# Kernel optimization log

Hardware: AMD Instinct MI355X
Metric: run time of the kernel (lower is better)

## Reference

```python
import jax, jax.numpy as jnp
import numpy as np

DT = 0.001          # continuous-dynamics step (dt > 0 branch)
KERNEL_SIZE = 16384 # L
P, H = 1024, 256    # d_state, d_input (= d_output)


def setup_inputs() -> dict:
    key = jax.random.key(0)
    kAr, kAi, kB, kC = jax.random.split(key, 4)
    # Continuous diagonal state matrix: real part in [strong, weak] = [-0.5, -0.01] (stable),
    # imaginary part uniform in [-pi, pi] (mimics diagonal_state_space_matrix init).
    Ar = jax.random.uniform(kAr, (P,), minval=-0.5, maxval=-0.01)
    Ai = jax.random.uniform(kAi, (P,), minval=-np.pi, maxval=np.pi)
    A = jnp.stack([Ar, Ai], axis=-1).astype(jnp.float32)            # (P, 2) view_as_real
    # B, C ~ uniform disk (radius 1): scaled complex gaussians are a fine stand-in numerically.
    B = (jax.random.normal(kB, (P, H, 2)) / np.sqrt(H)).astype(jnp.float32)   # (P, H, 2)
    C = (jax.random.normal(kC, (H, P, 2)) / np.sqrt(P)).astype(jnp.float32)   # (H, P, 2)
    return {"A": A, "B": B, "C": C}


def _as_complex(x):
    return x[..., 0] + 1j * x[..., 1]


def reference(A, B, C):
    """Vandermonde SSM kernel generation (continuous dt > 0 branch).
    Returns kernel (H, L, 2) = real view of complex kernel (H, L)."""
    Ac = _as_complex(A)   # (P,) complex
    Bc = _as_complex(B)   # (P, H)
    Cc = _as_complex(C)   # (H, P)

    # ZOH-style discretization
    A_bar = jnp.exp(Ac * DT)                               # (P,)
    B_bar = ((A_bar - 1.0) / Ac)[:, None] * Bc             # (P, H)

    # Vandermonde matrix V[p, l] = A_bar[p] ** l  (complex power == exp(l * log(a)))
    powers = jnp.arange(KERNEL_SIZE, dtype=jnp.float32)    # (L,)
    V = jnp.exp(jnp.log(A_bar)[:, None] * powers[None, :]) # (P, L)

    # W[h, p] = C[h, p] * B_bar[p, h]; kernel[h, l] = sum_p W[h, p] * V[p, l]
    W = Cc * B_bar.T                                       # (H, P)
    kernel = jnp.einsum('hp,pl->hl', W, V)                 # (H, L) complex
    return jnp.stack([kernel.real, kernel.imag], axis=-1)  # (H, L, 2) float32
```

## Files before the change

### kernel.cpp

```cpp
#include <hip/hip_runtime.h>
#include <hip/hip_fp16.h>

#define P_DIM 1024
#define H_DIM 256
#define L_DIM 16384
#define DT 0.001f
#define TWOPI 6.283185307179586f
#define WSCALE 4096.0f
#define INV_WSCALE (1.0f / 4096.0f)

#define BM 128
#define BN 128
#define BK 64
#define NTHREADS 256

typedef _Float16 f16x8 __attribute__((ext_vector_type(8)));
typedef float f32x4 __attribute__((ext_vector_type(4)));

#define GPTR(p) (const __attribute__((address_space(1))) unsigned*)(p)
#define LPTR(p) (__attribute__((address_space(3))) unsigned*)(p)

union H2U { __half2 h; unsigned u; };

__global__ __launch_bounds__(256)
void prep_kernel(const float* __restrict__ Ag, const float* __restrict__ Bg,
                 const float* __restrict__ Cg, __half* __restrict__ W2) {
    int gid = blockIdx.x * 256 + threadIdx.x;
    int h = gid >> 10, p = gid & 1023;
    float2 a = ((const float2*)Ag)[p];
    float er = __expf(a.x * DT);
    float s, c;
    __sincosf(a.y * DT, &s, &c);
    float nr = er * c - 1.0f, ni = er * s;
    float inv = 1.0f / (a.x * a.x + a.y * a.y);
    float sr = (nr * a.x + ni * a.y) * inv;
    float si = (ni * a.x - nr * a.y) * inv;
    float2 b = ((const float2*)Bg)[p * H_DIM + h];
    float2 cc = ((const float2*)Cg)[h * P_DIM + p];
    float tr = cc.x * sr - cc.y * si, ti = cc.x * si + cc.y * sr;
    float wr = (tr * b.x - ti * b.y) * WSCALE;
    float wi = (tr * b.y + ti * b.x) * WSCALE;
    ((__half2*)W2)[h * P_DIM + p] = __float22half2_rn(make_float2(wr, wi));
}

__global__ __launch_bounds__(NTHREADS)
void vand_mfma_kernel(const float* __restrict__ Ag,
                      const _Float16* __restrict__ W2,
                      float* __restrict__ out) {
    __shared__ __attribute__((aligned(16))) _Float16 As[BM * BK];
    __shared__ __attribute__((aligned(16))) _Float16 Bs[BN * BK];
    __shared__ __attribute__((aligned(16))) float2 pc[P_DIM];

    const int tid  = threadIdx.x;
    const int lane = tid & 63;
    const int w    = tid >> 6;
    const int wm   = w & 1;
    const int wn   = w >> 1;
    const int m0   = blockIdx.y * BM;
    const int nb   = blockIdx.x * BN;
    const int lb   = blockIdx.x * (BN / 2);

    #pragma unroll
    for (int i = 0; i < 4; ++i) {
        int p = i * 256 + tid;
        float2 a = ((const float2*)Ag)[p];
        pc[p] = make_float2(a.x * DT, a.y * DT * 0.15915494309189535f);
    }
    __syncthreads();

    f32x4 acc[4][4];
    #pragma unroll
    for (int mt = 0; mt < 4; ++mt)
        #pragma unroll
        for (int nt = 0; nt < 4; ++nt)
            acc[mt][nt] = (f32x4){0.f, 0.f, 0.f, 0.f};

    const int lv   = tid >> 2;
    const float fl = (float)(lb + lv);
    const int n0   = 2 * lv;
    const int qb   = tid & 3;

    for (int kk = 0; kk < 32; ++kk) {
        const int k0 = kk * BK;
        if (kk) __syncthreads();

        {
            const _Float16* gw = W2 + (size_t)(m0 + (w << 5)) * 2048 + k0;
            const int goff = (lane >> 3) * 2048 + (((lane & 7) ^ (lane >> 3)) << 3);
            _Float16* lbase = As + (w << 5) * 64;
            #pragma unroll
            for (int r = 0; r < 4; ++r) {
                __builtin_amdgcn_global_load_lds(GPTR(gw + r * 8 * 2048 + goff),
                                                 LPTR(lbase + r * 8 * 64), 16, 0, 0);
            }
        }

        #pragma unroll
        for (int i = 0; i < 4; ++i) {
            int q = qb + (i << 2);
            float4 pcv = *(const float4*)&pc[(k0 >> 1) + 2 * q];
            float mg0 = __expf(pcv.x * fl);
            float x0 = pcv.y * fl; x0 -= rintf(x0);
            float s0, c0; __sincosf(x0 * TWOPI, &s0, &c0);
            float vr0 = mg0 * c0, vi0 = mg0 * s0;
            float mg1 = __expf(pcv.z * fl);
            float x1 = pcv.w * fl; x1 -= rintf(x1);
            float s1, c1; __sincosf(x1 * TWOPI, &s1, &c1);
            float vr1 = mg1 * c1, vi1 = mg1 * s1;

            H2U a0, a1, b0, b1;
            a0.h = __float22half2_rn(make_float2(vr0, -vi0));
            a1.h = __float22half2_rn(make_float2(vr1, -vi1));
            b0.h = __float22half2_rn(make_float2(vi0, vr0));
            b1.h = __float22half2_rn(make_float2(vi1, vr1));
            int grp = q >> 1, sub = (q & 1) << 2;
            int e0 = n0 * 64 + ((grp ^ (n0 & 7)) << 3) + sub;
            int e1 = (n0 + 1) * 64 + ((grp ^ ((n0 + 1) & 7)) << 3) + sub;
            *(uint2*)(Bs + e0) = make_uint2(a0.u, a1.u);
            *(uint2*)(Bs + e1) = make_uint2(b0.u, b1.u);
        }
        __syncthreads();

        #pragma unroll
        for (int ks = 0; ks < 2; ++ks) {
            f16x8 af[4], bf[4];
            const int g = ks * 4 + (lane >> 4);
            #pragma unroll
            for (int t = 0; t < 4; ++t) {
                int m = wm * 64 + t * 16 + (lane & 15);
                af[t] = *(const f16x8*)(As + m * 64 + ((g ^ (m & 7)) << 3));
                int n = wn * 64 + t * 16 + (lane & 15);
                bf[t] = *(const f16x8*)(Bs + n * 64 + ((g ^ (n & 7)) << 3));
            }
            #pragma unroll
            for (int mt = 0; mt < 4; ++mt)
                #pragma unroll
                for (int nt = 0; nt < 4; ++nt)
                    acc[mt][nt] = __builtin_amdgcn_mfma_f32_16x16x32_f16(
                        af[mt], bf[nt], acc[mt][nt], 0, 0, 0);
        }
    }

    #pragma unroll
    for (int mt = 0; mt < 4; ++mt) {
        #pragma unroll
        for (int nt = 0; nt < 4; ++nt) {
            int h = m0 + wm * 64 + mt * 16 + ((lane >> 4) << 2);
            int n = nb + wn * 64 + nt * 16 + (lane & 15);
            #pragma unroll
            for (int r = 0; r < 4; ++r)
                out[(size_t)(h + r) * 32768 + n] = acc[mt][nt][r] * INV_WSCALE;
        }
    }
}

extern "C" void kernel_launch(void* const* d_in, const int* in_sizes, int n_in,
                              void* d_out, int out_size, void* d_ws, size_t ws_size,
                              hipStream_t stream) {
    const float* A = (const float*)d_in[0];
    const float* B = (const float*)d_in[1];
    const float* C = (const float*)d_in[2];
    float* out = (float*)d_out;
    __half* W2 = (__half*)d_ws;

    prep_kernel<<<dim3(1024), dim3(256), 0, stream>>>(A, B, C, W2);
    vand_mfma_kernel<<<dim3(L_DIM * 2 / BN, H_DIM / BM), dim3(NTHREADS), 0, stream>>>(
        A, (const _Float16*)W2, out);
}
```

Measured before the change: 115.6 us.

## Double-buffer LDS tiles, generate Vandermonde by recurrence, and tile prep transpose

The main kernel now double-buffers the A and B LDS tiles, so the next chunk's DMA and Vandermonde generation are issued before the current chunk's MFMAs, with one barrier per iteration. Each thread now computes one exp/sincos per state and derives three further consecutive powers by complex multiplication with A_bar, which reduces transcendental work per element. Launch bounds are raised to two blocks per CU. The prep kernel is restructured to load a block of B into shared memory so the transposed read is coalesced. The recurrence may accumulate rounding error, and the doubled LDS could limit occupancy.

```diff
diff --git a/kernel.cpp b/kernel.cpp
--- a/kernel.cpp
+++ b/kernel.cpp
@@ -6,13 +6,13 @@
 #define L_DIM 16384
 #define DT 0.001f
 #define TWOPI 6.283185307179586f
+#define INV2PI 0.15915494309189535f
 #define WSCALE 4096.0f
 #define INV_WSCALE (1.0f / 4096.0f)
-
 #define BM 128
 #define BN 128
 #define BK 64
-#define NTHREADS 256
+#define NT 256
 
 typedef _Float16 f16x8 __attribute__((ext_vector_type(8)));
 typedef float f32x4 __attribute__((ext_vector_type(4)));
@@ -21,52 +21,63 @@
 #define LPTR(p) (__attribute__((address_space(3))) unsigned*)(p)
 
 union H2U { __half2 h; unsigned u; };
+
+__device__ __forceinline__ float2 cmulf(float2 a, float2 b) {
+    return make_float2(a.x * b.x - a.y * b.y, a.x * b.y + a.y * b.x);
+}
 
 __global__ __launch_bounds__(256)
 void prep_kernel(const float* __restrict__ Ag, const float* __restrict__ Bg,
                  const float* __restrict__ Cg, __half* __restrict__ W2) {
-    int gid = blockIdx.x * 256 + threadIdx.x;
-    int h = gid >> 10, p = gid & 1023;
-    float2 a = ((const float2*)Ag)[p];
-    float er = __expf(a.x * DT);
-    float s, c;
-    __sincosf(a.y * DT, &s, &c);
-    float nr = er * c - 1.0f, ni = er * s;
-    float inv = 1.0f / (a.x * a.x + a.y * a.y);
-    float sr = (nr * a.x + ni * a.y) * inv;
-    float si = (ni * a.x - nr * a.y) * inv;
-    float2 b = ((const float2*)Bg)[p * H_DIM + h];
-    float2 cc = ((const float2*)Cg)[h * P_DIM + p];
-    float tr = cc.x * sr - cc.y * si, ti = cc.x * si + cc.y * sr;
-    float wr = (tr * b.x - ti * b.y) * WSCALE;
-    float wi = (tr * b.y + ti * b.x) * WSCALE;
-    ((__half2*)W2)[h * P_DIM + p] = __float22half2_rn(make_float2(wr, wi));
-}
-
-__global__ __launch_bounds__(NTHREADS)
+    __shared__ float2 Bt[64][33];
+    __shared__ float2 sc[64];
+    const int t  = threadIdx.x;
+    const int p0 = (blockIdx.x & 15) << 6;
+    const int h0 = (blockIdx.x >> 4) << 5;
+
+    if (t < 64) {
+        float2 a = ((const float2*)Ag)[p0 + t];
+        float er = __expf(a.x * DT);
+        float s, c; __sincosf(a.y * DT, &s, &c);
+        float nr = er * c - 1.f, ni = er * s;
+        float inv = 1.f / (a.x * a.x + a.y * a.y);
+        sc[t] = make_float2((nr * a.x + ni * a.y) * inv, (ni * a.x - nr * a.y) * inv);
+    }
+    #pragma unroll
+    for (int i = 0; i < 8; ++i) {
+        int idx = i * 256 + t, p = idx >> 5, h = idx & 31;
+        Bt[p][h] = ((const float2*)Bg)[(size_t)(p0 + p) * H_DIM + h0 + h];
+    }
+    __syncthreads();
+    #pragma unroll
+    for (int i = 0; i < 8; ++i) {
+        int idx = i * 256 + t, h = idx >> 6, p = idx & 63;
+        float2 cc = ((const float2*)Cg)[(size_t)(h0 + h) * P_DIM + p0 + p];
+        float2 s2 = sc[p], b = Bt[p][h0 ? h : h];
+        float2 tv = cmulf(cc, s2);
+        float wr = (tv.x * b.x - tv.y * b.y) * WSCALE;
+        float wi = (tv.x * b.y + tv.y * b.x) * WSCALE;
+        ((__half2*)W2)[(size_t)(h0 + h) * P_DIM + p0 + p] =
+            __float22half2_rn(make_float2(wr, wi));
+    }
+}
+
+__global__ __launch_bounds__(NT, 2)
 void vand_mfma_kernel(const float* __restrict__ Ag,
                       const _Float16* __restrict__ W2,
                       float* __restrict__ out) {
-    __shared__ __attribute__((aligned(16))) _Float16 As[BM * BK];
-    __shared__ __attribute__((aligned(16))) _Float16 Bs[BN * BK];
-    __shared__ __attribute__((aligned(16))) float2 pc[P_DIM];
+    __shared__ __attribute__((aligned(16))) _Float16 As[2][BM * BK];
+    __shared__ __attribute__((aligned(16))) _Float16 Bs[2][BN * BK];
 
     const int tid  = threadIdx.x;
     const int lane = tid & 63;
     const int w    = tid >> 6;
-    const int wm   = w & 1;
-    const int wn   = w >> 1;
+    const int wm   = w & 1, wn = w >> 1;
     const int m0   = blockIdx.y * BM;
     const int nb   = blockIdx.x * BN;
     const int lb   = blockIdx.x * (BN / 2);
 
-    #pragma unroll
-    for (int i = 0; i < 4; ++i) {
-        int p = i * 256 + tid;
-        float2 a = ((const float2*)Ag)[p];
-        pc[p] = make_float2(a.x * DT, a.y * DT * 0.15915494309189535f);
-    }
-    __syncthreads();
+    const float2* Ag2 = (const float2*)Ag;
 
     f32x4 acc[4][4];
     #pragma unroll
@@ -75,52 +86,71 @@
         for (int nt = 0; nt < 4; ++nt)
             acc[mt][nt] = (f32x4){0.f, 0.f, 0.f, 0.f};
 
-    const int lv   = tid >> 2;
-    const float fl = (float)(lb + lv);
-    const int n0   = 2 * lv;
-    const int qb   = tid & 3;
+    const int q    = tid & 15;
+    const int llq  = (tid >> 4) << 2;
+    const float l0f = (float)(lb + llq);
+    const int grp  = q >> 1, sub = (q & 1) << 2;
+
+    const int goff = (lane >> 3) * 2048 + (((lane & 7) ^ (lane >> 3)) << 3);
+    const _Float16* gwbase = W2 + (size_t)(m0 + (w << 5)) * 2048;
+    const int ldsoff = (w << 5) * 64;
+
+    _Float16* Acur = &As[0][0]; _Float16* Bcur = &Bs[0][0];
+    _Float16* Anxt = &As[1][0]; _Float16* Bnxt = &Bs[1][0];
+
+#define DMA_CHUNK(K0, DST)                                                        \
+    {                                                                             \
+        const _Float16* gw = gwbase + (K0) + goff;                                \
+        _Float16* lB = (DST) + ldsoff;                                            \
+        _Pragma("unroll")                                                         \
+        for (int r = 0; r < 4; ++r)                                               \
+            __builtin_amdgcn_global_load_lds(GPTR(gw + r * 8 * 2048),             \
+                                             LPTR(lB + r * 8 * 64), 16, 0, 0);    \
+    }
+
+#define VGEN_CHUNK(K0, DST)                                                       \
+    {                                                                             \
+        float2 a0 = Ag2[((K0) >> 1) + 2 * q];                                     \
+        float2 a1 = Ag2[((K0) >> 1) + 2 * q + 1];                                 \
+        float c0x = a0.x * DT, c0y = a0.y * (DT * INV2PI);                        \
+        float c1x = a1.x * DT, c1y = a1.y * (DT * INV2PI);                        \
+        float s, c;                                                               \
+        float e0 = __expf(c0x); __sincosf(c0y * TWOPI, &s, &c);                   \
+        float2 ab0 = make_float2(e0 * c, e0 * s);                                 \
+        float e1 = __expf(c1x); __sincosf(c1y * TWOPI, &s, &c);                   \
+        float2 ab1 = make_float2(e1 * c, e1 * s);                                 \
+        float mg = __expf(c0x * l0f);                                             \
+        float x = c0y * l0f; x -= rintf(x); __sincosf(x * TWOPI, &s, &c);         \
+        float2 v0 = make_float2(mg * c, mg * s);                                  \
+        mg = __expf(c1x * l0f);                                                   \
+        x = c1y * l0f; x -= rintf(x); __sincosf(x * TWOPI, &s, &c);               \
+        float2 v1 = make_float2(mg * c, mg * s);                                  \
+        _Pragma("unroll")                                                         \
+        for (int j = 0; j < 4; ++j) {                                             \
+            int n0 = 2 * (llq + j);                                               \
+            H2U h0u, h1u, h2u, h3u;                                               \
+            h0u.h = __float22half2_rn(make_float2(v0.x, -v0.y));                  \
+            h1u.h = __float22half2_rn(make_float2(v1.x, -v1.y));                  \
+            h2u.h = __float22half2_rn(make_float2(v0.y, v0.x));                   \
+            h3u.h = __float22half2_rn(make_float2(v1.y, v1.x));                   \
+            int e0i = n0 * 64 + ((grp ^ (n0 & 7)) << 3) + sub;                    \
+            int e1i = (n0 + 1) * 64 + ((grp ^ ((n0 + 1) & 7)) << 3) + sub;        \
+            *(uint2*)((DST) + e0i) = make_uint2(h0u.u, h1u.u);                    \
+            *(uint2*)((DST) + e1i) = make_uint2(h2u.u, h3u.u);                    \
+            if (j < 3) { v0 = cmulf(v0, ab0); v1 = cmulf(v1, ab1); }              \
+        }                                                                         \
+    }
+
+    DMA_CHUNK(0, Acur)
+    VGEN_CHUNK(0, Bcur)
+    __syncthreads();
 
     for (int kk = 0; kk < 32; ++kk) {
-        const int k0 = kk * BK;
-        if (kk) __syncthreads();
-
-        {
-            const _Float16* gw = W2 + (size_t)(m0 + (w << 5)) * 2048 + k0;
-            const int goff = (lane >> 3) * 2048 + (((lane & 7) ^ (lane >> 3)) << 3);
-            _Float16* lbase = As + (w << 5) * 64;
-            #pragma unroll
-            for (int r = 0; r < 4; ++r) {
-                __builtin_amdgcn_global_load_lds(GPTR(gw + r * 8 * 2048 + goff),
-                                                 LPTR(lbase + r * 8 * 64), 16, 0, 0);
-            }
+        if (kk < 31) {
+            const int k1 = (kk + 1) * BK;
+            DMA_CHUNK(k1, Anxt)
+            VGEN_CHUNK(k1, Bnxt)
         }
-
-        #pragma unroll
-        for (int i = 0; i < 4; ++i) {
-            int q = qb + (i << 2);
-            float4 pcv = *(const float4*)&pc[(k0 >> 1) + 2 * q];
-            float mg0 = __expf(pcv.x * fl);
-            float x0 = pcv.y * fl; x0 -= rintf(x0);
-            float s0, c0; __sincosf(x0 * TWOPI, &s0, &c0);
-            float vr0 = mg0 * c0, vi0 = mg0 * s0;
-            float mg1 = __expf(pcv.z * fl);
-            float x1 = pcv.w * fl; x1 -= rintf(x1);
-            float s1, c1; __sincosf(x1 * TWOPI, &s1, &c1);
-            float vr1 = mg1 * c1, vi1 = mg1 * s1;
-
-            H2U a0, a1, b0, b1;
-            a0.h = __float22half2_rn(make_float2(vr0, -vi0));
-            a1.h = __float22half2_rn(make_float2(vr1, -vi1));
-            b0.h = __float22half2_rn(make_float2(vi0, vr0));
-            b1.h = __float22half2_rn(make_float2(vi1, vr1));
-            int grp = q >> 1, sub = (q & 1) << 2;
-            int e0 = n0 * 64 + ((grp ^ (n0 & 7)) << 3) + sub;
-            int e1 = (n0 + 1) * 64 + ((grp ^ ((n0 + 1) & 7)) << 3) + sub;
-            *(uint2*)(Bs + e0) = make_uint2(a0.u, a1.u);
-            *(uint2*)(Bs + e1) = make_uint2(b0.u, b1.u);
-        }
-        __syncthreads();
-
         #pragma unroll
         for (int ks = 0; ks < 2; ++ks) {
             f16x8 af[4], bf[4];
@@ -128,9 +158,9 @@
             #pragma unroll
             for (int t = 0; t < 4; ++t) {
                 int m = wm * 64 + t * 16 + (lane & 15);
-                af[t] = *(const f16x8*)(As + m * 64 + ((g ^ (m & 7)) << 3));
+                af[t] = *(const f16x8*)(Acur + m * 64 + ((g ^ (m & 7)) << 3));
                 int n = wn * 64 + t * 16 + (lane & 15);
-                bf[t] = *(const f16x8*)(Bs + n * 64 + ((g ^ (n & 7)) << 3));
+                bf[t] = *(const f16x8*)(Bcur + n * 64 + ((g ^ (n & 7)) << 3));
             }
             #pragma unroll
             for (int mt = 0; mt < 4; ++mt)
@@ -139,6 +169,9 @@
                     acc[mt][nt] = __builtin_amdgcn_mfma_f32_16x16x32_f16(
                         af[mt], bf[nt], acc[mt][nt], 0, 0, 0);
         }
+        __syncthreads();
+        _Float16* tA = Acur; Acur = Anxt; Anxt = tA;
+        _Float16* tB = Bcur; Bcur = Bnxt; Bnxt = tB;
     }
 
     #pragma unroll
@@ -152,6 +185,8 @@
                 out[(size_t)(h + r) * 32768 + n] = acc[mt][nt][r] * INV_WSCALE;
         }
     }
+#undef DMA_CHUNK
+#undef VGEN_CHUNK
 }
 
 extern "C" void kernel_launch(void* const* d_in, const int* in_sizes, int n_in,
@@ -163,7 +198,7 @@
     float* out = (float*)d_out;
     __half* W2 = (__half*)d_ws;
 
-    prep_kernel<<<dim3(1024), dim3(256), 0, stream>>>(A, B, C, W2);
-    vand_mfma_kernel<<<dim3(L_DIM * 2 / BN, H_DIM / BM), dim3(NTHREADS), 0, stream>>>(
+    prep_kernel<<<dim3(128), dim3(256), 0, stream>>>(A, B, C, W2);
+    vand_mfma_kernel<<<dim3(L_DIM * 2 / BN, H_DIM / BM), dim3(NT), 0, stream>>>(
         A, (const _Float16*)W2, out);
 }
```

Result: faster. 111.8 us (-3.3%).
